# Kernel tuning notes

Measured on AMD Instinct MI355X. Metric: run time of the kernel, lower is better.

Reference implementation:

```python
import jax, jax.numpy as jnp
import numpy as np

B, S, D, H = 16, 512, 1024, 16
DH = D // H  # 64


def setup_inputs() -> dict:
    key = jax.random.key(0)
    kx, kq, kk, kv = jax.random.split(key, 4)
    stdv = 1.0 / np.sqrt(DH)  # reset_param uses 1/sqrt(t.size(1)) = 1/sqrt(head_dim)
    x = jax.random.normal(kx, (B, S, D), dtype=jnp.float32)
    Wq = jax.random.uniform(kq, (H, D, DH), dtype=jnp.float32, minval=-stdv, maxval=stdv)
    Wk = jax.random.uniform(kk, (H, D, DH), dtype=jnp.float32, minval=-stdv, maxval=stdv)
    Wv = jax.random.uniform(kv, (H, D, DH), dtype=jnp.float32, minval=-stdv, maxval=stdv)
    return {"x": x, "Wq": Wq, "Wk": Wk, "Wv": Wv}


def reference(x, Wq, Wk, Wv):
    # x: [B, S, D]; Wq/Wk/Wv: [H, D, DH] (stacked per-head params)
    q = jnp.einsum('bsd,hde->bhse', x, Wq)  # [B,H,S,DH]
    k = jnp.einsum('bsd,hde->bhse', x, Wk)
    v = jnp.einsum('bsd,hde->bhse', x, Wv)
    # NOTE: original scales by sqrt(input_dim), not sqrt(head_dim)
    scale = 1.0 / jnp.sqrt(jnp.float32(D))
    scores = jnp.einsum('bhse,bhte->bhst', q, k) * scale  # [B,H,S,S]
    attn = jax.nn.softmax(scores, axis=-1)
    out = jnp.einsum('bhst,bhte->bhse', attn, v)  # [B,H,S,DH]
    # concat heads along feature dim (head order matches torch cat over loop)
    return out.transpose(0, 2, 1, 3).reshape(x.shape[0], x.shape[1], D)
```

## Files before the change

### kernel.cpp

```cpp
#include <hip/hip_runtime.h>
#include <math.h>

constexpr int B = 16, S = 512, D = 1024, H = 16, DH = 64;
constexpr int BH = B * H;

typedef short bf16x8 __attribute__((ext_vector_type(8)));
typedef float f32x4  __attribute__((ext_vector_type(4)));

__device__ __forceinline__ unsigned short f2bf(float f) {
    unsigned u = __float_as_uint(f);
    u += 0x7fff + ((u >> 16) & 1);
    return (unsigned short)(u >> 16);
}

#define VMC0  asm volatile("s_waitcnt vmcnt(0)" ::: "memory")
#define BARR  __builtin_amdgcn_s_barrier()

__global__ __launch_bounds__(256) void convert_x(
    const float* __restrict__ x, unsigned short* __restrict__ xb)
{
    int i = blockIdx.x * 256 + threadIdx.x;
    float4 v = ((const float4*)x)[i];
    ushort4 o;
    o.x = f2bf(v.x); o.y = f2bf(v.y); o.z = f2bf(v.z); o.w = f2bf(v.w);
    ((ushort4*)xb)[i] = o;
}

__global__ __launch_bounds__(256) void convert_w(
    const float* __restrict__ Wq, const float* __restrict__ Wk,
    const float* __restrict__ Wv, unsigned short* __restrict__ WbT)
{
    __shared__ float tile[64][65];
    const int d0 = blockIdx.x * 64;
    const int h = blockIdx.y, m = blockIdx.z;
    const float* W = ((m == 0) ? Wq : (m == 1) ? Wk : Wv) + (size_t)h * D * DH;
    const int t = threadIdx.x;
    {
        int e = t & 63, dr = t >> 6;
        #pragma unroll
        for (int i = 0; i < 16; ++i) {
            int d = dr * 16 + i;
            tile[d][e] = W[(size_t)(d0 + d) * DH + e];
        }
    }
    __syncthreads();
    {
        int d = t & 63, er = t >> 6;
        unsigned short* out = WbT + (size_t)(m * H + h) * DH * D;
        #pragma unroll
        for (int i = 0; i < 16; ++i) {
            int e = er * 16 + i;
            out[(size_t)e * D + d0 + d] = f2bf(tile[d][e]);
        }
    }
}

__global__ __launch_bounds__(256) void qkv_gemm(
    const unsigned short* __restrict__ xb,
    const unsigned short* __restrict__ WbT,
    unsigned short* __restrict__ qkvb)
{
    __shared__ unsigned short As[128 * 64];
    __shared__ unsigned short Bs[128 * 64];

    const int t = threadIdx.x;
    const int w = t >> 6;
    const int wr = w >> 1, wc = w & 1;
    const int L = t & 63;
    const int lane15 = L & 15;
    const int quad = L >> 4;
    const int lrow8 = L >> 3;
    const int lg = L & 7;

    const int r0 = blockIdx.x * 128;
    const int n0 = blockIdx.y * 128;

    f32x4 acc[4][4] = {};

    for (int k0 = 0; k0 < D; k0 += 64) {
        #pragma unroll
        for (int i = 0; i < 4; ++i) {
            int c = w * 4 + i;
            int r = c * 8 + lrow8;
            int gg = lg ^ (r & 7);
            const unsigned short* gp = xb + (size_t)(r0 + r) * D + k0 + gg * 8;
            __builtin_amdgcn_global_load_lds(
                (const __attribute__((address_space(1))) void*)gp,
                (__attribute__((address_space(3))) void*)(As + c * 512),
                16, 0, 0);
            const unsigned short* gq = WbT + (size_t)(n0 + r) * D + k0 + gg * 8;
            __builtin_amdgcn_global_load_lds(
                (const __attribute__((address_space(1))) void*)gq,
                (__attribute__((address_space(3))) void*)(Bs + c * 512),
                16, 0, 0);
        }
        __syncthreads();

        #pragma unroll
        for (int ks = 0; ks < 2; ++ks) {
            int gk = ks * 4 + quad;
            bf16x8 a[4], bb[4];
            #pragma unroll
            for (int rt = 0; rt < 4; ++rt) {
                int ml = wr * 64 + rt * 16 + lane15;
                a[rt] = *(const bf16x8*)(As + ml * 64 + ((gk ^ (ml & 7)) * 8));
            }
            #pragma unroll
            for (int ct = 0; ct < 4; ++ct) {
                int nl = wc * 64 + ct * 16 + lane15;
                bb[ct] = *(const bf16x8*)(Bs + nl * 64 + ((gk ^ (nl & 7)) * 8));
            }
            #pragma unroll
            for (int rt = 0; rt < 4; ++rt)
                #pragma unroll
                for (int ct = 0; ct < 4; ++ct)
                    acc[rt][ct] = __builtin_amdgcn_mfma_f32_16x16x32_bf16(
                        a[rt], bb[ct], acc[rt][ct], 0, 0, 0);
        }
        __syncthreads();
    }

    const int m  = n0 >> 10;
    const int h  = ((n0 >> 6) + wc) & 15;
    const int bb_ = r0 >> 9;
    const int s0 = (r0 & 511) + wr * 64;

    if (m == 2) {
        unsigned short* outv = qkvb + ((size_t)(2 * BH) + (bb_ * H + h)) * (size_t)(S * DH);
        #pragma unroll
        for (int rt = 0; rt < 4; ++rt) {
            int srow = s0 + rt * 16 + quad * 4;
            #pragma unroll
            for (int ct = 0; ct < 4; ++ct) {
                int e = ct * 16 + lane15;
                ushort4 pk;
                pk.x = f2bf(acc[rt][ct][0]);
                pk.y = f2bf(acc[rt][ct][1]);
                pk.z = f2bf(acc[rt][ct][2]);
                pk.w = f2bf(acc[rt][ct][3]);
                *(ushort4*)(outv + (size_t)e * S + srow) = pk;
            }
        }
    } else {
        const float sc = (m == 0) ? 0.04508422002778011f : 1.0f;
        unsigned short* out = qkvb + ((size_t)m * BH + (bb_ * H + h)) * (size_t)(S * DH);
        #pragma unroll
        for (int rt = 0; rt < 4; ++rt) {
            #pragma unroll
            for (int ct = 0; ct < 4; ++ct) {
                int e = ct * 16 + lane15;
                #pragma unroll
                for (int r = 0; r < 4; ++r) {
                    int srow = s0 + rt * 16 + quad * 4 + r;
                    out[(size_t)srow * DH + e] = f2bf(acc[rt][ct][r] * sc);
                }
            }
        }
    }
}

__global__ __launch_bounds__(512) void attn_mfma(
    const unsigned short* __restrict__ qkvb, float* __restrict__ out)
{
    __shared__ unsigned short Qs[256 * 64];
    __shared__ unsigned short KsA[8 * 64 * 64];
    __shared__ unsigned short VtA[8 * 64 * 64];

    const int t = threadIdx.x;
    const int w = t >> 6;
    const int L = t & 63;
    const int lane15 = L & 15;
    const int quad = L >> 4;
    const int lrow8 = L >> 3;
    const int lg = L & 7;
    const int qr0 = blockIdx.x * 256;
    const int bh = blockIdx.y;
    const int b = bh >> 4, h = bh & 15;

    const unsigned short* qb = qkvb + (size_t)bh * S * DH;
    const unsigned short* kb = qkvb + (size_t)(BH + bh) * S * DH;
    const unsigned short* vt = qkvb + (size_t)(2 * BH + bh) * S * DH;

    #pragma unroll
    for (int i = 0; i < 4; ++i) {
        int base = i * 64 + w * 8;
        int r = base + lrow8;
        int gg = lg ^ (r & 7);
        __builtin_amdgcn_global_load_lds(
            (const __attribute__((address_space(1))) void*)
                (qb + (size_t)(qr0 + r) * DH + gg * 8),
            (__attribute__((address_space(3))) void*)(Qs + base * 64),
            16, 0, 0);
    }
    #pragma unroll
    for (int tt = 0; tt < 8; ++tt) {
        int base = w * 8;
        int r = base + lrow8;
        int gr = (r & 32) | ((r & 12) << 1) | ((r & 16) >> 2) | (r & 3);
        int gg = lg ^ (r & 7);
        __builtin_amdgcn_global_load_lds(
            (const __attribute__((address_space(1))) void*)
                (kb + (size_t)(tt * 64 + gr) * DH + gg * 8),
            (__attribute__((address_space(3))) void*)(KsA + tt * 4096 + base * 64),
            16, 0, 0);
        __builtin_amdgcn_global_load_lds(
            (const __attribute__((address_space(1))) void*)
                (vt + (size_t)r * S + tt * 64 + gg * 8),
            (__attribute__((address_space(3))) void*)(VtA + tt * 4096 + base * 64),
            16, 0, 0);
    }
    VMC0;
    BARR;

    bf16x8 qf[2][2];
    #pragma unroll
    for (int mt = 0; mt < 2; ++mt)
        #pragma unroll
        for (int ks = 0; ks < 2; ++ks) {
            int ml = w * 32 + mt * 16 + lane15;
            int gk = ks * 4 + quad;
            qf[mt][ks] = *(const bf16x8*)(Qs + ml * 64 + ((gk ^ (lane15 & 7)) * 8));
        }

    f32x4 o[2][4] = {};
    float plsum[2] = {0.f, 0.f};

    #pragma unroll 2
    for (int tt = 0; tt < 8; ++tt) {
        const unsigned short* Kt = KsA + tt * 4096;
        const unsigned short* Vt = VtA + tt * 4096;

        bf16x8 kf[2][4], vf[2][4];
        #pragma unroll
        for (int ks = 0; ks < 2; ++ks) {
            int gk = ks * 4 + quad;
            #pragma unroll
            for (int ct = 0; ct < 4; ++ct) {
                int kr = ct * 16 + lane15;
                kf[ks][ct] = *(const bf16x8*)(Kt + kr * 64 + ((gk ^ (lane15 & 7)) * 8));
                vf[ks][ct] = *(const bf16x8*)(Vt + kr * 64 + ((gk ^ (lane15 & 7)) * 8));
            }
        }

        f32x4 st[2][4] = {};
        __builtin_amdgcn_s_setprio(1);
        #pragma unroll
        for (int ks = 0; ks < 2; ++ks)
            #pragma unroll
            for (int mt = 0; mt < 2; ++mt)
                #pragma unroll
                for (int ct = 0; ct < 4; ++ct)
                    st[mt][ct] = __builtin_amdgcn_mfma_f32_16x16x32_bf16(
                        kf[ks][ct], qf[mt][ks], st[mt][ct], 0, 0, 0);
        __builtin_amdgcn_s_setprio(0);

        bf16x8 pB[2][2];
        #pragma unroll
        for (int mt = 0; mt < 2; ++mt) {
            float rs = 0.f;
            union { unsigned u[4]; bf16x8 v; } pu[2];
            #pragma unroll
            for (int ct = 0; ct < 4; ++ct) {
                float p0 = exp2f(st[mt][ct][0]);
                float p1 = exp2f(st[mt][ct][1]);
                float p2 = exp2f(st[mt][ct][2]);
                float p3 = exp2f(st[mt][ct][3]);
                rs += (p0 + p1) + (p2 + p3);
                unsigned lo, hi;
                asm("v_cvt_pk_bf16_f32 %0, %1, %2" : "=v"(lo) : "v"(p0), "v"(p1));
                asm("v_cvt_pk_bf16_f32 %0, %1, %2" : "=v"(hi) : "v"(p2), "v"(p3));
                pu[ct >> 1].u[(ct & 1) * 2 + 0] = lo;
                pu[ct >> 1].u[(ct & 1) * 2 + 1] = hi;
            }
            pB[mt][0] = pu[0].v;
            pB[mt][1] = pu[1].v;
            plsum[mt] += rs;
        }

        __builtin_amdgcn_s_setprio(1);
        #pragma unroll
        for (int ks = 0; ks < 2; ++ks)
            #pragma unroll
            for (int mt = 0; mt < 2; ++mt)
                #pragma unroll
                for (int nt = 0; nt < 4; ++nt)
                    o[mt][nt] = __builtin_amdgcn_mfma_f32_16x16x32_bf16(
                        vf[ks][nt], pB[mt][ks], o[mt][nt], 0, 0, 0);
        __builtin_amdgcn_s_setprio(0);
    }

    #pragma unroll
    for (int mt = 0; mt < 2; ++mt) {
        float l = plsum[mt];
        l += __shfl_xor(l, 16, 64);
        l += __shfl_xor(l, 32, 64);
        float inv = 1.0f / l;
        int srow = qr0 + w * 32 + mt * 16 + lane15;
        float* op = out + (size_t)(b * S + srow) * D + h * DH;
        #pragma unroll
        for (int nt = 0; nt < 4; ++nt) {
            float4 v;
            v.x = o[mt][nt][0] * inv;
            v.y = o[mt][nt][1] * inv;
            v.z = o[mt][nt][2] * inv;
            v.w = o[mt][nt][3] * inv;
            *(float4*)(op + nt * 16 + quad * 4) = v;
        }
    }
}

extern "C" void kernel_launch(void* const* d_in, const int* in_sizes, int n_in,
                              void* d_out, int out_size, void* d_ws, size_t ws_size,
                              hipStream_t stream) {
    const float* x  = (const float*)d_in[0];
    const float* Wq = (const float*)d_in[1];
    const float* Wk = (const float*)d_in[2];
    const float* Wv = (const float*)d_in[3];
    float* outp = (float*)d_out;

    unsigned short* qkvb = (unsigned short*)d_ws;
    unsigned short* xb   = (unsigned short*)((char*)d_ws + 50331648);
    unsigned short* WbT  = (unsigned short*)((char*)d_ws + 67108864);

    convert_x<<<dim3((B * S * D / 4) / 256), 256, 0, stream>>>(x, xb);
    convert_w<<<dim3(D / 64, H, 3), 256, 0, stream>>>(Wq, Wk, Wv, WbT);
    qkv_gemm<<<dim3(B * S / 128, 3 * H * DH / 128), 256, 0, stream>>>(xb, WbT, qkvb);
    attn_mfma<<<dim3(S / 256, BH), 512, 0, stream>>>(qkvb, outp);
}
```

Before: 196.7 us.

## Stream K/V tiles through double-buffered LDS and fuse conversion kernels

The attention kernel no longer stages the whole K/V head in shared memory. It streams 64-row K/V tiles through a small double buffer and halves the query rows per block, which doubles the grid and cuts shared memory use so several blocks can share a CU. The separate x and weight conversion kernels are merged into one launch to save a kernel launch. In exchange, each tile step adds a barrier and global-load wait, and each wave now does less MFMA work per K/V fragment load.

```diff
diff --git a/kernel.cpp b/kernel.cpp
--- a/kernel.cpp
+++ b/kernel.cpp
@@ -14,27 +14,32 @@
 }
 
 #define VMC0  asm volatile("s_waitcnt vmcnt(0)" ::: "memory")
+#define LGKM0 asm volatile("s_waitcnt lgkmcnt(0)" ::: "memory")
 #define BARR  __builtin_amdgcn_s_barrier()
 
-__global__ __launch_bounds__(256) void convert_x(
-    const float* __restrict__ x, unsigned short* __restrict__ xb)
-{
-    int i = blockIdx.x * 256 + threadIdx.x;
-    float4 v = ((const float4*)x)[i];
-    ushort4 o;
-    o.x = f2bf(v.x); o.y = f2bf(v.y); o.z = f2bf(v.z); o.w = f2bf(v.w);
-    ((ushort4*)xb)[i] = o;
-}
-
-__global__ __launch_bounds__(256) void convert_w(
+__global__ __launch_bounds__(256) void convert_all(
+    const float* __restrict__ x, unsigned short* __restrict__ xb,
     const float* __restrict__ Wq, const float* __restrict__ Wk,
     const float* __restrict__ Wv, unsigned short* __restrict__ WbT)
 {
     __shared__ float tile[64][65];
-    const int d0 = blockIdx.x * 64;
-    const int h = blockIdx.y, m = blockIdx.z;
+    const int t = threadIdx.x;
+    const int bx = blockIdx.x;
+
+    if (bx < 8192) {
+        int i = bx * 256 + t;
+        float4 v = ((const float4*)x)[i];
+        ushort4 o;
+        o.x = f2bf(v.x); o.y = f2bf(v.y); o.z = f2bf(v.z); o.w = f2bf(v.w);
+        ((ushort4*)xb)[i] = o;
+        return;
+    }
+
+    const int cw = bx - 8192;
+    const int d0 = (cw & 15) * 64;
+    const int h = (cw >> 4) & 15;
+    const int m = cw >> 8;
     const float* W = ((m == 0) ? Wq : (m == 1) ? Wk : Wv) + (size_t)h * D * DH;
-    const int t = threadIdx.x;
     {
         int e = t & 63, dr = t >> 6;
         #pragma unroll
@@ -159,12 +164,11 @@
     }
 }
 
-__global__ __launch_bounds__(512) void attn_mfma(
+__global__ __launch_bounds__(512, 4) void attn_mfma(
     const unsigned short* __restrict__ qkvb, float* __restrict__ out)
 {
-    __shared__ unsigned short Qs[256 * 64];
-    __shared__ unsigned short KsA[8 * 64 * 64];
-    __shared__ unsigned short VtA[8 * 64 * 64];
+    __shared__ unsigned short KV[2][2][64 * 64];
+    unsigned short* Qs = &KV[0][0][0];
 
     const int t = threadIdx.x;
     const int w = t >> 6;
@@ -173,7 +177,7 @@
     const int quad = L >> 4;
     const int lrow8 = L >> 3;
     const int lg = L & 7;
-    const int qr0 = blockIdx.x * 256;
+    const int qr0 = blockIdx.x * 128;
     const int bh = blockIdx.y;
     const int b = bh >> 4, h = bh & 15;
 
@@ -182,8 +186,8 @@
     const unsigned short* vt = qkvb + (size_t)(2 * BH + bh) * S * DH;
 
     #pragma unroll
-    for (int i = 0; i < 4; ++i) {
-        int base = i * 64 + w * 8;
+    for (int p = 0; p < 2; ++p) {
+        int base = p * 64 + w * 8;
         int r = base + lrow8;
         int gg = lg ^ (r & 7);
         __builtin_amdgcn_global_load_lds(
@@ -192,79 +196,74 @@
             (__attribute__((address_space(3))) void*)(Qs + base * 64),
             16, 0, 0);
     }
+    VMC0;
+    BARR;
+
+    bf16x8 qf[2];
     #pragma unroll
-    for (int tt = 0; tt < 8; ++tt) {
-        int base = w * 8;
-        int r = base + lrow8;
+    for (int ks = 0; ks < 2; ++ks) {
+        int ml = w * 16 + lane15;
+        int gk = ks * 4 + quad;
+        qf[ks] = *(const bf16x8*)(Qs + ml * 64 + ((gk ^ (lane15 & 7)) * 8));
+    }
+    LGKM0;
+    BARR;
+
+    {
+        int r = w * 8 + lrow8;
         int gr = (r & 32) | ((r & 12) << 1) | ((r & 16) >> 2) | (r & 3);
         int gg = lg ^ (r & 7);
         __builtin_amdgcn_global_load_lds(
             (const __attribute__((address_space(1))) void*)
-                (kb + (size_t)(tt * 64 + gr) * DH + gg * 8),
-            (__attribute__((address_space(3))) void*)(KsA + tt * 4096 + base * 64),
+                (kb + (size_t)gr * DH + gg * 8),
+            (__attribute__((address_space(3))) void*)(&KV[0][0][0] + (w * 8) * 64),
             16, 0, 0);
         __builtin_amdgcn_global_load_lds(
             (const __attribute__((address_space(1))) void*)
-                (vt + (size_t)r * S + tt * 64 + gg * 8),
-            (__attribute__((address_space(3))) void*)(VtA + tt * 4096 + base * 64),
+                (vt + (size_t)r * S + gg * 8),
+            (__attribute__((address_space(3))) void*)(&KV[0][1][0] + (w * 8) * 64),
             16, 0, 0);
     }
     VMC0;
     BARR;
 
-    bf16x8 qf[2][2];
-    #pragma unroll
-    for (int mt = 0; mt < 2; ++mt)
-        #pragma unroll
-        for (int ks = 0; ks < 2; ++ks) {
-            int ml = w * 32 + mt * 16 + lane15;
-            int gk = ks * 4 + quad;
-            qf[mt][ks] = *(const bf16x8*)(Qs + ml * 64 + ((gk ^ (lane15 & 7)) * 8));
-        }
-
-    f32x4 o[2][4] = {};
-    float plsum[2] = {0.f, 0.f};
+    f32x4 o[4] = {};
+    float plsum = 0.f;
 
     #pragma unroll 2
-    for (int tt = 0; tt < 8; ++tt) {
-        const unsigned short* Kt = KsA + tt * 4096;
-        const unsigned short* Vt = VtA + tt * 4096;
-
-        bf16x8 kf[2][4], vf[2][4];
+    for (int kt = 0; kt < 8; ++kt) {
+        const int cur = kt & 1;
+        const unsigned short* Kt  = &KV[cur][0][0];
+        const unsigned short* Vtl = &KV[cur][1][0];
+
+        f32x4 st[4] = {};
         #pragma unroll
         for (int ks = 0; ks < 2; ++ks) {
             int gk = ks * 4 + quad;
+            bf16x8 kf[4];
             #pragma unroll
             for (int ct = 0; ct < 4; ++ct) {
                 int kr = ct * 16 + lane15;
-                kf[ks][ct] = *(const bf16x8*)(Kt + kr * 64 + ((gk ^ (lane15 & 7)) * 8));
-                vf[ks][ct] = *(const bf16x8*)(Vt + kr * 64 + ((gk ^ (lane15 & 7)) * 8));
-            }
-        }
-
-        f32x4 st[2][4] = {};
-        __builtin_amdgcn_s_setprio(1);
-        #pragma unroll
-        for (int ks = 0; ks < 2; ++ks)
-            #pragma unroll
-            for (int mt = 0; mt < 2; ++mt)
-                #pragma unroll
-                for (int ct = 0; ct < 4; ++ct)
-                    st[mt][ct] = __builtin_amdgcn_mfma_f32_16x16x32_bf16(
-                        kf[ks][ct], qf[mt][ks], st[mt][ct], 0, 0, 0);
-        __builtin_amdgcn_s_setprio(0);
-
-        bf16x8 pB[2][2];
-        #pragma unroll
-        for (int mt = 0; mt < 2; ++mt) {
+                kf[ct] = *(const bf16x8*)(Kt + kr * 64 + ((gk ^ (lane15 & 7)) * 8));
+            }
+            __builtin_amdgcn_s_setprio(1);
+            #pragma unroll
+            for (int ct = 0; ct < 4; ++ct)
+                st[ct] = __builtin_amdgcn_mfma_f32_16x16x32_bf16(
+                    kf[ct], qf[ks], st[ct], 0, 0, 0);
+            __builtin_amdgcn_s_setprio(0);
+        }
+
+        bf16x8 pB[2];
+        {
             float rs = 0.f;
             union { unsigned u[4]; bf16x8 v; } pu[2];
             #pragma unroll
             for (int ct = 0; ct < 4; ++ct) {
-                float p0 = exp2f(st[mt][ct][0]);
-                float p1 = exp2f(st[mt][ct][1]);
-                float p2 = exp2f(st[mt][ct][2]);
-                float p3 = exp2f(st[mt][ct][3]);
+                float p0 = exp2f(st[ct][0]);
+                float p1 = exp2f(st[ct][1]);
+                float p2 = exp2f(st[ct][2]);
+                float p3 = exp2f(st[ct][3]);
                 rs += (p0 + p1) + (p2 + p3);
                 unsigned lo, hi;
                 asm("v_cvt_pk_bf16_f32 %0, %1, %2" : "=v"(lo) : "v"(p0), "v"(p1));
@@ -272,38 +271,62 @@
                 pu[ct >> 1].u[(ct & 1) * 2 + 0] = lo;
                 pu[ct >> 1].u[(ct & 1) * 2 + 1] = hi;
             }
-            pB[mt][0] = pu[0].v;
-            pB[mt][1] = pu[1].v;
-            plsum[mt] += rs;
-        }
-
-        __builtin_amdgcn_s_setprio(1);
-        #pragma unroll
-        for (int ks = 0; ks < 2; ++ks)
-            #pragma unroll
-            for (int mt = 0; mt < 2; ++mt)
-                #pragma unroll
-                for (int nt = 0; nt < 4; ++nt)
-                    o[mt][nt] = __builtin_amdgcn_mfma_f32_16x16x32_bf16(
-                        vf[ks][nt], pB[mt][ks], o[mt][nt], 0, 0, 0);
-        __builtin_amdgcn_s_setprio(0);
-    }
-
-    #pragma unroll
-    for (int mt = 0; mt < 2; ++mt) {
-        float l = plsum[mt];
+            pB[0] = pu[0].v;
+            pB[1] = pu[1].v;
+            plsum += rs;
+        }
+
+        #pragma unroll
+        for (int ks = 0; ks < 2; ++ks) {
+            int gk = ks * 4 + quad;
+            bf16x8 vf[4];
+            #pragma unroll
+            for (int nt = 0; nt < 4; ++nt) {
+                int dh = nt * 16 + lane15;
+                vf[nt] = *(const bf16x8*)(Vtl + dh * 64 + ((gk ^ (lane15 & 7)) * 8));
+            }
+            __builtin_amdgcn_s_setprio(1);
+            #pragma unroll
+            for (int nt = 0; nt < 4; ++nt)
+                o[nt] = __builtin_amdgcn_mfma_f32_16x16x32_bf16(
+                    vf[nt], pB[ks], o[nt], 0, 0, 0);
+            __builtin_amdgcn_s_setprio(0);
+        }
+
+        if (kt < 7) {
+            int r = w * 8 + lrow8;
+            int gr = (r & 32) | ((r & 12) << 1) | ((r & 16) >> 2) | (r & 3);
+            int gg = lg ^ (r & 7);
+            int kn = (kt + 1) * 64;
+            __builtin_amdgcn_global_load_lds(
+                (const __attribute__((address_space(1))) void*)
+                    (kb + (size_t)(kn + gr) * DH + gg * 8),
+                (__attribute__((address_space(3))) void*)(&KV[cur ^ 1][0][0] + (w * 8) * 64),
+                16, 0, 0);
+            __builtin_amdgcn_global_load_lds(
+                (const __attribute__((address_space(1))) void*)
+                    (vt + (size_t)r * S + kn + gg * 8),
+                (__attribute__((address_space(3))) void*)(&KV[cur ^ 1][1][0] + (w * 8) * 64),
+                16, 0, 0);
+            VMC0;
+            BARR;
+        }
+    }
+
+    {
+        float l = plsum;
         l += __shfl_xor(l, 16, 64);
         l += __shfl_xor(l, 32, 64);
         float inv = 1.0f / l;
-        int srow = qr0 + w * 32 + mt * 16 + lane15;
+        int srow = qr0 + w * 16 + lane15;
         float* op = out + (size_t)(b * S + srow) * D + h * DH;
         #pragma unroll
         for (int nt = 0; nt < 4; ++nt) {
             float4 v;
-            v.x = o[mt][nt][0] * inv;
-            v.y = o[mt][nt][1] * inv;
-            v.z = o[mt][nt][2] * inv;
-            v.w = o[mt][nt][3] * inv;
+            v.x = o[nt][0] * inv;
+            v.y = o[nt][1] * inv;
+            v.z = o[nt][2] * inv;
+            v.w = o[nt][3] * inv;
             *(float4*)(op + nt * 16 + quad * 4) = v;
         }
     }
@@ -322,8 +345,7 @@
     unsigned short* xb   = (unsigned short*)((char*)d_ws + 50331648);
     unsigned short* WbT  = (unsigned short*)((char*)d_ws + 67108864);
 
-    convert_x<<<dim3((B * S * D / 4) / 256), 256, 0, stream>>>(x, xb);
-    convert_w<<<dim3(D / 64, H, 3), 256, 0, stream>>>(Wq, Wk, Wv, WbT);
+    convert_all<<<dim3(8192 + 768), 256, 0, stream>>>(x, xb, Wq, Wk, Wv, WbT);
     qkv_gemm<<<dim3(B * S / 128, 3 * H * DH / 128), 256, 0, stream>>>(xb, WbT, qkvb);
-    attn_mfma<<<dim3(S / 256, BH), 512, 0, stream>>>(qkvb, outp);
-}
+    attn_mfma<<<dim3(S / 128, BH), 512, 0, stream>>>(qkvb, outp);
+}
```

Measured after the change: 193.0 us. Within noise of the previous version (-1.9%).
